# Performance work log

Hardware: AMD Instinct MI355X
Metric: run time of the kernel (lower is better)

## Reference

```python
import jax, jax.numpy as jnp
from jax import lax
import numpy as np

T, B, I, H, L = 512, 256, 512, 256, 2  # seq, batch, input, hidden, layers per stack


def _param_shapes():
    # (stack, layer) -> input dim of that layer. Stack1 layer0 sees I, everything else sees H.
    shapes = []
    for s, in0 in enumerate([I, H]):
        for l in range(L):
            d_in = in0 if l == 0 else H
            shapes.append((f"s{s+1}l{l}", d_in))
    return shapes


def setup_inputs() -> dict:
    key = jax.random.key(0)
    d = {"x": jax.random.normal(jax.random.fold_in(key, 0), (T, B, I), jnp.float32)}
    k = 1.0 / np.sqrt(H)  # pytorch LSTM init scale
    i = 1
    for name, d_in in _param_shapes():
        d[name + "_wih"] = jax.random.uniform(jax.random.fold_in(key, i + 0), (4 * H, d_in), jnp.float32, -k, k)
        d[name + "_whh"] = jax.random.uniform(jax.random.fold_in(key, i + 1), (4 * H, H), jnp.float32, -k, k)
        d[name + "_bih"] = jax.random.uniform(jax.random.fold_in(key, i + 2), (4 * H,), jnp.float32, -k, k)
        d[name + "_bhh"] = jax.random.uniform(jax.random.fold_in(key, i + 3), (4 * H,), jnp.float32, -k, k)
        i += 4
    d["lr_w"] = jax.random.uniform(jax.random.fold_in(key, 100), (H, H), jnp.float32, -k, k)
    d["lr_b"] = jax.random.uniform(jax.random.fold_in(key, 101), (H,), jnp.float32, -k, k)
    return d


def _lstm_layer(x, wih, whh, bih, bhh):
    # x: (T, B, d_in) -> (T, B, H). PyTorch gate order: i, f, g, o.
    xg = jnp.einsum("tbi,gi->tbg", x, wih) + bih + bhh  # precompute input proj (T, B, 4H)
    h0 = jnp.zeros((x.shape[1], H), x.dtype)

    def step(carry, xt):
        h, c = carry
        g = xt + h @ whh.T
        gi, gf, gg, go = jnp.split(g, 4, axis=-1)
        c = jax.nn.sigmoid(gf) * c + jax.nn.sigmoid(gi) * jnp.tanh(gg)
        h = jax.nn.sigmoid(go) * jnp.tanh(c)
        return (h, c), h

    _, ys = lax.scan(step, (h0, h0), xg)
    return ys


def _forward(x, params, lr_w, lr_b):
    out = x
    for (wih, whh, bih, bhh) in params:
        out = _lstm_layer(out, wih, whh, bih, bhh)
    out = out @ lr_w.T + lr_b  # (T, B, H)
    return out[:, -1]  # faithful to original: index dim 1 (batch dim) -> (T, H)


def reference(x,
              s1l0_wih, s1l0_whh, s1l0_bih, s1l0_bhh,
              s1l1_wih, s1l1_whh, s1l1_bih, s1l1_bhh,
              s2l0_wih, s2l0_whh, s2l0_bih, s2l0_bhh,
              s2l1_wih, s2l1_whh, s2l1_bih, s2l1_bhh,
              lr_w, lr_b):
    params = [
        (s1l0_wih, s1l0_whh, s1l0_bih, s1l0_bhh),
        (s1l1_wih, s1l1_whh, s1l1_bih, s1l1_bhh),
        (s2l0_wih, s2l0_whh, s2l0_bih, s2l0_bhh),
        (s2l1_wih, s2l1_whh, s2l1_bih, s2l1_bhh),
    ]
    return _forward(x, params, lr_w, lr_b)
```

## Files before the change

### kernel.cpp

```cpp
#include <hip/hip_runtime.h>
#include <stdint.h>


typedef _Float16 half2v __attribute__((ext_vector_type(2)));

__device__ __forceinline__ float fdot2u(uint32_t w, uint32_t h, float acc) {
#if __has_builtin(__builtin_amdgcn_fdot2)
  return __builtin_amdgcn_fdot2(__builtin_bit_cast(half2v, w),
                                __builtin_bit_cast(half2v, h), acc, false);
#else
  half2v wv = __builtin_bit_cast(half2v, w);
  half2v hv = __builtin_bit_cast(half2v, h);
  acc += (float)wv[0] * (float)hv[0];
  acc += (float)wv[1] * (float)hv[1];
  return acc;
#endif
}

__device__ __forceinline__ float sigmoidf_(float x) {
  return 1.f / (1.f + __expf(-x));
}
__device__ __forceinline__ float tanhf_(float x) {
  return 1.f - 2.f / (__expf(2.f * x) + 1.f);
}

#define CNT_STRIDE 32

__device__ __forceinline__ int cnt_load(const int* p) {
  return __hip_atomic_load(p, __ATOMIC_RELAXED, __HIP_MEMORY_SCOPE_AGENT);
}
__device__ __forceinline__ void cnt_store(int* p, int v) {
  __hip_atomic_store(p, v, __ATOMIC_RELAXED, __HIP_MEMORY_SCOPE_AGENT);
}
__device__ __forceinline__ float ldg_f32(const float* p) {
  uint32_t u = __hip_atomic_load((const uint32_t*)p, __ATOMIC_RELAXED,
                                 __HIP_MEMORY_SCOPE_AGENT);
  return __builtin_bit_cast(float, u);
}
__device__ __forceinline__ void stg_f32(float* p, float v) {
  __hip_atomic_store((uint32_t*)p, __builtin_bit_cast(uint32_t, v),
                     __ATOMIC_RELAXED, __HIP_MEMORY_SCOPE_AGENT);
}
__device__ __forceinline__ uint64_t ldg_u64(const float* p) {
  return __hip_atomic_load((const uint64_t*)p, __ATOMIC_RELAXED,
                           __HIP_MEMORY_SCOPE_AGENT);
}

__device__ __forceinline__ void wait_ge(const int* p, int need, int& rdy) {
  while (rdy < need) {
    rdy = cnt_load(p);
    if (rdy < need) __builtin_amdgcn_s_sleep(2);
  }
  asm volatile("" ::: "memory");
}

__global__ void zero_cnt(int* c) {
  if (threadIdx.x < 16 * CNT_STRIDE) c[threadIdx.x] = 0;
}

__global__ __launch_bounds__(256) void pack_whh(const float* __restrict__ w,
                                                uint32_t* __restrict__ wpk) {
  int idx = blockIdx.x * 256 + threadIdx.x;
  int r = idx >> 7, k2 = idx & 127;
  float f0 = w[r * 256 + 2 * k2];
  float f1 = w[r * 256 + 2 * k2 + 1];
  union { _Float16 h; uint16_t u; } a, b;
  a.h = (_Float16)f0;
  b.h = (_Float16)f1;
  wpk[idx] = (uint32_t)a.u | ((uint32_t)b.u << 16);
}

__global__ __launch_bounds__(256) void proj_gemm(const float* __restrict__ in, int istride, int K,
                                                 const float* __restrict__ W,
                                                 const float* __restrict__ bih,
                                                 const float* __restrict__ bhh,
                                                 float* __restrict__ xg) {
  __shared__ float xs[8][512];
  const int tid = threadIdx.x;
  const int r = blockIdx.x * 256 + tid;
  const int t0 = blockIdx.y * 8;
  for (int tt = 0; tt < 8; ++tt)
    for (int k = tid; k < K; k += 256)
      xs[tt][k] = in[(size_t)(t0 + tt) * istride + k];
  __syncthreads();
  float bias = bih[r] + bhh[r];
  float acc[8];
#pragma unroll
  for (int j = 0; j < 8; ++j) acc[j] = bias;
  const float* wr = W + (size_t)r * K;
  for (int k = 0; k < K; k += 4) {
    float4 w4 = *reinterpret_cast<const float4*>(wr + k);
#pragma unroll
    for (int j = 0; j < 8; ++j)
      acc[j] += xs[j][k] * w4.x + xs[j][k + 1] * w4.y + xs[j][k + 2] * w4.z +
                xs[j][k + 3] * w4.w;
  }
#pragma unroll
  for (int j = 0; j < 8; ++j) xg[(size_t)(t0 + j) * 1024 + r] = acc[j];
}


__device__ void scan_fn(int l, const uint32_t* __restrict__ wpk,
                        const float* __restrict__ xgsrc,
                        float* __restrict__ hseq, int* __restrict__ cnt) {
  __shared__ __align__(16) uint4 wlds[8 * 2 * 512];
  __shared__ __align__(16) uint16_t hbuf[2][256];
  const int tid = threadIdx.x;
  const int j = tid >> 1;
  const int odd = tid & 1;
  const int rA = j + (odd ? 512 : 0);
  const int rB = rA + 256;

  uint32_t wA[96], wB[96];
  {
    const uint4* gA = reinterpret_cast<const uint4*>(wpk + rA * 128);
    const uint4* gB = reinterpret_cast<const uint4*>(wpk + rB * 128);
#pragma unroll
    for (int q = 0; q < 24; ++q) {
      uint4 a = gA[q];
      wA[4 * q + 0] = a.x; wA[4 * q + 1] = a.y; wA[4 * q + 2] = a.z; wA[4 * q + 3] = a.w;
      uint4 b = gB[q];
      wB[4 * q + 0] = b.x; wB[4 * q + 1] = b.y; wB[4 * q + 2] = b.z; wB[4 * q + 3] = b.w;
    }
#pragma unroll
    for (int c = 0; c < 8; ++c) {
      wlds[(c * 2 + 0) * 512 + tid] = gA[24 + c];
      wlds[(c * 2 + 1) * 512 + tid] = gB[24 + c];
    }
  }
  if (tid < 256) hbuf[0][tid] = 0;
  __syncthreads();

  const int* mycnt = &cnt[(4 + (l - 1) * 2 + odd) * CNT_STRIDE];
  int rdy = 0;
  if (l) wait_ge(mycnt, 1, rdy);
  float c_ = 0.f;
  float xga = ldg_f32(xgsrc + rA), xgb = ldg_f32(xgsrc + rB);
  int pp = 0;
  for (int t = 0; t < 512; ++t) {
    const int tn = (t < 511) ? (t + 1) : 511;
    if (l) {
      int need = (t + 2 > 512) ? 512 : (t + 2);
      wait_ge(mycnt, need, rdy);
    }
    float nxa = ldg_f32(xgsrc + tn * 1024 + rA);
    float nxb = ldg_f32(xgsrc + tn * 1024 + rB);

    float accA0 = xga, accA1 = 0.f, accB0 = xgb, accB1 = 0.f;
    const uint4* hv4 = reinterpret_cast<const uint4*>(&hbuf[pp][0]);
#pragma unroll
    for (int ch = 0; ch < 24; ++ch) {
      uint4 h4 = hv4[ch];
      accA0 = fdot2u(wA[4 * ch + 0], h4.x, accA0);
      accA1 = fdot2u(wA[4 * ch + 1], h4.y, accA1);
      accA0 = fdot2u(wA[4 * ch + 2], h4.z, accA0);
      accA1 = fdot2u(wA[4 * ch + 3], h4.w, accA1);
      accB0 = fdot2u(wB[4 * ch + 0], h4.x, accB0);
      accB1 = fdot2u(wB[4 * ch + 1], h4.y, accB1);
      accB0 = fdot2u(wB[4 * ch + 2], h4.z, accB0);
      accB1 = fdot2u(wB[4 * ch + 3], h4.w, accB1);
    }
#pragma unroll
    for (int cc = 0; cc < 8; ++cc) {
      uint4 h4 = hv4[24 + cc];
      uint4 wa = wlds[(cc * 2 + 0) * 512 + tid];
      uint4 wb = wlds[(cc * 2 + 1) * 512 + tid];
      accA0 = fdot2u(wa.x, h4.x, accA0);
      accA1 = fdot2u(wa.y, h4.y, accA1);
      accA0 = fdot2u(wa.z, h4.z, accA0);
      accA1 = fdot2u(wa.w, h4.w, accA1);
      accB0 = fdot2u(wb.x, h4.x, accB0);
      accB1 = fdot2u(wb.y, h4.y, accB1);
      accB0 = fdot2u(wb.z, h4.z, accB0);
      accB1 = fdot2u(wb.w, h4.w, accB1);
    }
    float accA = accA0 + accA1;
    float accB = accB0 + accB1;

    float o0 = __shfl_xor(accA, 1);
    float o1 = __shfl_xor(accB, 1);
    float pi = odd ? o0 : accA;
    float pf = odd ? o1 : accB;
    float pg = odd ? accA : o0;
    float po = odd ? accB : o1;

    c_ = sigmoidf_(pf) * c_ + sigmoidf_(pi) * tanhf_(pg);
    float h = sigmoidf_(po) * tanhf_(c_);
    if (!odd) {
      stg_f32(hseq + t * 256 + j, h);
      union { _Float16 hf; uint16_t u; } cv;
      cv.hf = (_Float16)h;
      hbuf[pp ^ 1][j] = cv.u;
    }
    __syncthreads();
    if (tid == 0) cnt_store(&cnt[l * CNT_STRIDE], t + 1);
    pp ^= 1;
    xga = nxa;
    xgb = nxb;
  }
}

__device__ void proj_fn(int l, int half, const uint32_t* __restrict__ wpk,
                        const float* __restrict__ bih, const float* __restrict__ bhh,
                        const float* __restrict__ hsrc,
                        float* __restrict__ xgdst, int* __restrict__ cnt) {
  __shared__ __align__(16) uint32_t hpk[128];
  const int tid = threadIdx.x;
  const int row = half * 512 + tid;

  uint32_t wr_[128];
  {
    const uint4* g = reinterpret_cast<const uint4*>(wpk + (size_t)row * 128);
#pragma unroll
    for (int q = 0; q < 32; ++q) {
      uint4 v = g[q];
      wr_[4 * q + 0] = v.x; wr_[4 * q + 1] = v.y; wr_[4 * q + 2] = v.z; wr_[4 * q + 3] = v.w;
    }
  }
  const float bias = bih[row] + bhh[row];
  const int* prev = &cnt[(l - 1) * CNT_STRIDE];
  int* mine = &cnt[(4 + (l - 1) * 2 + half) * CNT_STRIDE];
  int rdy = 0;

  for (int t = 0; t < 512; ++t) {
    wait_ge(prev, t + 1, rdy);
    if (tid < 128) {
      uint64_t hv = ldg_u64(hsrc + t * 256 + 2 * tid);
      float hx = __builtin_bit_cast(float, (uint32_t)hv);
      float hy = __builtin_bit_cast(float, (uint32_t)(hv >> 32));
      union { _Float16 h; uint16_t u; } a, b;
      a.h = (_Float16)hx;
      b.h = (_Float16)hy;
      hpk[tid] = (uint32_t)a.u | ((uint32_t)b.u << 16);
    }
    __syncthreads();
    float a0 = bias, a1 = 0.f;
    const uint4* hv4 = reinterpret_cast<const uint4*>(hpk);
#pragma unroll
    for (int q = 0; q < 32; ++q) {
      uint4 h4 = hv4[q];
      a0 = fdot2u(wr_[4 * q + 0], h4.x, a0);
      a1 = fdot2u(wr_[4 * q + 1], h4.y, a1);
      a0 = fdot2u(wr_[4 * q + 2], h4.z, a0);
      a1 = fdot2u(wr_[4 * q + 3], h4.w, a1);
    }
    stg_f32(xgdst + t * 1024 + row, a0 + a1);
    __syncthreads();
    if (tid == 0) cnt_store(mine, t + 1);
  }
}

__global__ __launch_bounds__(512, 2) void pipeline(
    const uint32_t* __restrict__ wpkhh, const uint32_t* __restrict__ wpkih,
    const float* __restrict__ xg0, float* __restrict__ xgp,
    float* __restrict__ hseq,
    const float* __restrict__ bih1, const float* __restrict__ bhh1,
    const float* __restrict__ bih2, const float* __restrict__ bhh2,
    const float* __restrict__ bih3, const float* __restrict__ bhh3,
    int* __restrict__ cnt) {
  const int bx = blockIdx.x;
  if (bx == 0) {
    scan_fn(0, wpkhh, xg0, hseq, cnt);
  } else {
    const int g = bx - 1;
    const int l = g / 3 + 1;
    const int r = g % 3;
    const float* bih = (l == 1) ? bih1 : (l == 2) ? bih2 : bih3;
    const float* bhh = (l == 1) ? bhh1 : (l == 2) ? bhh2 : bhh3;
    if (r < 2)
      proj_fn(l, r, wpkih + (size_t)(l - 1) * 131072, bih, bhh,
              hseq + (size_t)(l - 1) * 131072, xgp + (size_t)(l - 1) * 524288, cnt);
    else
      scan_fn(l, wpkhh + (size_t)l * 131072, xgp + (size_t)(l - 1) * 524288,
              hseq + (size_t)l * 131072, cnt);
  }
}

__global__ __launch_bounds__(256) void final_gemm(const float* __restrict__ h3,
                                                  const float* __restrict__ lrw,
                                                  const float* __restrict__ lrb,
                                                  float* __restrict__ out) {
  __shared__ float xs[8][256];
  const int j = threadIdx.x;
  const int t0 = blockIdx.x * 8;
  for (int tt = 0; tt < 8; ++tt) xs[tt][j] = h3[(t0 + tt) * 256 + j];
  __syncthreads();
  float bias = lrb[j];
  float acc[8];
#pragma unroll
  for (int jj = 0; jj < 8; ++jj) acc[jj] = bias;
  const float* wr = lrw + j * 256;
  for (int k = 0; k < 256; k += 4) {
    float4 w4 = *reinterpret_cast<const float4*>(wr + k);
#pragma unroll
    for (int jj = 0; jj < 8; ++jj)
      acc[jj] += xs[jj][k] * w4.x + xs[jj][k + 1] * w4.y + xs[jj][k + 2] * w4.z +
                 xs[jj][k + 3] * w4.w;
  }
#pragma unroll
  for (int jj = 0; jj < 8; ++jj) out[(t0 + jj) * 256 + j] = acc[jj];
}

extern "C" void kernel_launch(void* const* d_in, const int* in_sizes, int n_in,
                              void* d_out, int out_size, void* d_ws, size_t ws_size,
                              hipStream_t stream) {
  (void)in_sizes; (void)n_in; (void)out_size; (void)ws_size;
  const float* x = (const float*)d_in[0];
  const float* wih[4] = {(const float*)d_in[1], (const float*)d_in[5],
                         (const float*)d_in[9], (const float*)d_in[13]};
  const float* whh[4] = {(const float*)d_in[2], (const float*)d_in[6],
                         (const float*)d_in[10], (const float*)d_in[14]};
  const float* bih[4] = {(const float*)d_in[3], (const float*)d_in[7],
                         (const float*)d_in[11], (const float*)d_in[15]};
  const float* bhh[4] = {(const float*)d_in[4], (const float*)d_in[8],
                         (const float*)d_in[12], (const float*)d_in[16]};
  const float* lrw = (const float*)d_in[17];
  const float* lrb = (const float*)d_in[18];
  float* out = (float*)d_out;

  float* ws = (float*)d_ws;
  float* xg0 = ws;
  float* xgp = ws + 524288;
  float* hseq = xgp + 3 * 524288;
  uint32_t* wpkhh = (uint32_t*)(hseq + 4 * 131072);
  uint32_t* wpkih = wpkhh + 4 * 131072;
  int* cnt = (int*)(wpkih + 3 * 131072);

  zero_cnt<<<1, 512, 0, stream>>>(cnt);
  for (int l = 0; l < 4; ++l)
    pack_whh<<<512, 256, 0, stream>>>(whh[l], wpkhh + (size_t)l * 131072);
  for (int l = 1; l < 4; ++l)
    pack_whh<<<512, 256, 0, stream>>>(wih[l], wpkih + (size_t)(l - 1) * 131072);

  proj_gemm<<<dim3(4, 64), 256, 0, stream>>>(x + 255 * 512, 256 * 512, 512,
                                             wih[0], bih[0], bhh[0], xg0);

  pipeline<<<10, 512, 0, stream>>>(wpkhh, wpkih, xg0, xgp, hseq,
                                   bih[1], bhh[1], bih[2], bhh[2], bih[3], bhh[3],
                                   cnt);

  final_gemm<<<64, 256, 0, stream>>>(hseq + 3 * 131072, lrw, lrb, out);
}
```

Measured before the change: 1.176 ms.

## Fuse final linear into pipeline, batch projection steps by four, merge pack kernels

Merges the seven weight-pack launches into one kernel that picks its source matrix by block index. Projection blocks now wait for four timesteps at a time and compute four outputs per synchronisation, which cuts counter polling and barrier overhead. The final linear layer moves into an extra pipeline block that consumes the last layer's hidden states as they are produced, so it overlaps the scan instead of running after it. The cost is more latency between a scan step and its consumer, and one more persistent block spinning on counters.

```diff
diff --git a/kernel.cpp b/kernel.cpp
--- a/kernel.cpp
+++ b/kernel.cpp
@@ -58,16 +58,24 @@
   if (threadIdx.x < 16 * CNT_STRIDE) c[threadIdx.x] = 0;
 }
 
-__global__ __launch_bounds__(256) void pack_whh(const float* __restrict__ w,
-                                                uint32_t* __restrict__ wpk) {
-  int idx = blockIdx.x * 256 + threadIdx.x;
+__global__ __launch_bounds__(256) void pack_all(
+    const float* __restrict__ w0, const float* __restrict__ w1,
+    const float* __restrict__ w2, const float* __restrict__ w3,
+    const float* __restrict__ w4, const float* __restrict__ w5,
+    const float* __restrict__ w6, uint32_t* __restrict__ dst) {
+  int b = blockIdx.x;
+  int m = b >> 9;
+  const float* src = (m == 0) ? w0 : (m == 1) ? w1 : (m == 2) ? w2
+                   : (m == 3) ? w3 : (m == 4) ? w4 : (m == 5) ? w5 : w6;
+  uint32_t* d = dst + (size_t)m * 131072;
+  int idx = (b & 511) * 256 + threadIdx.x;
   int r = idx >> 7, k2 = idx & 127;
-  float f0 = w[r * 256 + 2 * k2];
-  float f1 = w[r * 256 + 2 * k2 + 1];
-  union { _Float16 h; uint16_t u; } a, b;
+  float f0 = src[r * 256 + 2 * k2];
+  float f1 = src[r * 256 + 2 * k2 + 1];
+  union { _Float16 h; uint16_t u; } a, bb;
   a.h = (_Float16)f0;
-  b.h = (_Float16)f1;
-  wpk[idx] = (uint32_t)a.u | ((uint32_t)b.u << 16);
+  bb.h = (_Float16)f1;
+  d[idx] = (uint32_t)a.u | ((uint32_t)bb.u << 16);
 }
 
 __global__ __launch_bounds__(256) void proj_gemm(const float* __restrict__ in, int istride, int K,
@@ -204,7 +212,7 @@
                         const float* __restrict__ bih, const float* __restrict__ bhh,
                         const float* __restrict__ hsrc,
                         float* __restrict__ xgdst, int* __restrict__ cnt) {
-  __shared__ __align__(16) uint32_t hpk[128];
+  __shared__ __align__(16) uint32_t hpk[4][128];
   const int tid = threadIdx.x;
   const int row = half * 512 + tid;
 
@@ -221,32 +229,79 @@
   const int* prev = &cnt[(l - 1) * CNT_STRIDE];
   int* mine = &cnt[(4 + (l - 1) * 2 + half) * CNT_STRIDE];
   int rdy = 0;
-
-  for (int t = 0; t < 512; ++t) {
-    wait_ge(prev, t + 1, rdy);
-    if (tid < 128) {
-      uint64_t hv = ldg_u64(hsrc + t * 256 + 2 * tid);
+  const int s4 = tid >> 7;
+  const int c4 = tid & 127;
+
+  for (int tt = 0; tt < 128; ++tt) {
+    const int t0 = tt * 4;
+    wait_ge(prev, t0 + 4, rdy);
+    {
+      uint64_t hv = ldg_u64(hsrc + (t0 + s4) * 256 + 2 * c4);
       float hx = __builtin_bit_cast(float, (uint32_t)hv);
       float hy = __builtin_bit_cast(float, (uint32_t)(hv >> 32));
       union { _Float16 h; uint16_t u; } a, b;
       a.h = (_Float16)hx;
       b.h = (_Float16)hy;
-      hpk[tid] = (uint32_t)a.u | ((uint32_t)b.u << 16);
-    }
-    __syncthreads();
-    float a0 = bias, a1 = 0.f;
-    const uint4* hv4 = reinterpret_cast<const uint4*>(hpk);
+      hpk[s4][c4] = (uint32_t)a.u | ((uint32_t)b.u << 16);
+    }
+    __syncthreads();
+#pragma unroll
+    for (int s = 0; s < 4; ++s) {
+      float a0 = bias, a1 = 0.f;
+      const uint4* hv4 = reinterpret_cast<const uint4*>(hpk[s]);
+#pragma unroll
+      for (int q = 0; q < 32; ++q) {
+        uint4 h4 = hv4[q];
+        a0 = fdot2u(wr_[4 * q + 0], h4.x, a0);
+        a1 = fdot2u(wr_[4 * q + 1], h4.y, a1);
+        a0 = fdot2u(wr_[4 * q + 2], h4.z, a0);
+        a1 = fdot2u(wr_[4 * q + 3], h4.w, a1);
+      }
+      stg_f32(xgdst + (t0 + s) * 1024 + row, a0 + a1);
+    }
+    __syncthreads();
+    if (tid == 0) cnt_store(mine, t0 + 4);
+  }
+}
+
+__device__ void final_fn(const float* __restrict__ lrw, const float* __restrict__ lrb,
+                         const float* __restrict__ h3, float* __restrict__ out,
+                         const int* __restrict__ cnt) {
+  __shared__ __align__(16) float hs[256];
+  const int tid = threadIdx.x;
+  const int row = tid >> 1;
+  const int kh = tid & 1;
+  float w_[128];
+  {
+    const float4* g = reinterpret_cast<const float4*>(lrw + (size_t)row * 256 + kh * 128);
 #pragma unroll
     for (int q = 0; q < 32; ++q) {
-      uint4 h4 = hv4[q];
-      a0 = fdot2u(wr_[4 * q + 0], h4.x, a0);
-      a1 = fdot2u(wr_[4 * q + 1], h4.y, a1);
-      a0 = fdot2u(wr_[4 * q + 2], h4.z, a0);
-      a1 = fdot2u(wr_[4 * q + 3], h4.w, a1);
-    }
-    stg_f32(xgdst + t * 1024 + row, a0 + a1);
-    __syncthreads();
-    if (tid == 0) cnt_store(mine, t + 1);
+      float4 v = g[q];
+      w_[4 * q + 0] = v.x; w_[4 * q + 1] = v.y; w_[4 * q + 2] = v.z; w_[4 * q + 3] = v.w;
+    }
+  }
+  const float bias = lrb[row];
+  const int* prev = &cnt[3 * CNT_STRIDE];
+  int rdy = 0;
+  for (int t = 0; t < 512; ++t) {
+    wait_ge(prev, t + 1, rdy);
+    if (tid < 128) {
+      uint64_t hv = ldg_u64(h3 + t * 256 + 2 * tid);
+      hs[2 * tid] = __builtin_bit_cast(float, (uint32_t)hv);
+      hs[2 * tid + 1] = __builtin_bit_cast(float, (uint32_t)(hv >> 32));
+    }
+    __syncthreads();
+    float a0 = 0.f, a1 = 0.f;
+    const float* hp = hs + kh * 128;
+#pragma unroll
+    for (int k = 0; k < 128; k += 4) {
+      a0 += w_[k] * hp[k] + w_[k + 2] * hp[k + 2];
+      a1 += w_[k + 1] * hp[k + 1] + w_[k + 3] * hp[k + 3];
+    }
+    float s = a0 + a1;
+    s += __shfl_xor(s, 1);
+    if (!kh) out[t * 256 + row] = s + bias;
+    __syncthreads();
   }
 }
 
@@ -257,10 +312,13 @@
     const float* __restrict__ bih1, const float* __restrict__ bhh1,
     const float* __restrict__ bih2, const float* __restrict__ bhh2,
     const float* __restrict__ bih3, const float* __restrict__ bhh3,
-    int* __restrict__ cnt) {
+    const float* __restrict__ lrw, const float* __restrict__ lrb,
+    float* __restrict__ out, int* __restrict__ cnt) {
   const int bx = blockIdx.x;
   if (bx == 0) {
     scan_fn(0, wpkhh, xg0, hseq, cnt);
+  } else if (bx == 10) {
+    final_fn(lrw, lrb, hseq + (size_t)3 * 131072, out, cnt);
   } else {
     const int g = bx - 1;
     const int l = g / 3 + 1;
@@ -274,31 +332,6 @@
       scan_fn(l, wpkhh + (size_t)l * 131072, xgp + (size_t)(l - 1) * 524288,
               hseq + (size_t)l * 131072, cnt);
   }
-}
-
-__global__ __launch_bounds__(256) void final_gemm(const float* __restrict__ h3,
-                                                  const float* __restrict__ lrw,
-                                                  const float* __restrict__ lrb,
-                                                  float* __restrict__ out) {
-  __shared__ float xs[8][256];
-  const int j = threadIdx.x;
-  const int t0 = blockIdx.x * 8;
-  for (int tt = 0; tt < 8; ++tt) xs[tt][j] = h3[(t0 + tt) * 256 + j];
-  __syncthreads();
-  float bias = lrb[j];
-  float acc[8];
-#pragma unroll
-  for (int jj = 0; jj < 8; ++jj) acc[jj] = bias;
-  const float* wr = lrw + j * 256;
-  for (int k = 0; k < 256; k += 4) {
-    float4 w4 = *reinterpret_cast<const float4*>(wr + k);
-#pragma unroll
-    for (int jj = 0; jj < 8; ++jj)
-      acc[jj] += xs[jj][k] * w4.x + xs[jj][k + 1] * w4.y + xs[jj][k + 2] * w4.z +
-                 xs[jj][k + 3] * w4.w;
-  }
-#pragma unroll
-  for (int jj = 0; jj < 8; ++jj) out[(t0 + jj) * 256 + j] = acc[jj];
 }
 
 extern "C" void kernel_launch(void* const* d_in, const int* in_sizes, int n_in,
@@ -327,17 +360,13 @@
   int* cnt = (int*)(wpkih + 3 * 131072);
 
   zero_cnt<<<1, 512, 0, stream>>>(cnt);
-  for (int l = 0; l < 4; ++l)
-    pack_whh<<<512, 256, 0, stream>>>(whh[l], wpkhh + (size_t)l * 131072);
-  for (int l = 1; l < 4; ++l)
-    pack_whh<<<512, 256, 0, stream>>>(wih[l], wpkih + (size_t)(l - 1) * 131072);
+  pack_all<<<3584, 256, 0, stream>>>(whh[0], whh[1], whh[2], whh[3],
+                                     wih[1], wih[2], wih[3], wpkhh);
 
   proj_gemm<<<dim3(4, 64), 256, 0, stream>>>(x + 255 * 512, 256 * 512, 512,
                                              wih[0], bih[0], bhh[0], xg0);
 
-  pipeline<<<10, 512, 0, stream>>>(wpkhh, wpkih, xg0, xgp, hseq,
+  pipeline<<<11, 512, 0, stream>>>(wpkhh, wpkih, xg0, xgp, hseq,
                                    bih[1], bhh[1], bih[2], bhh[2], bih[3], bhh[3],
-                                   cnt);
-
-  final_gemm<<<64, 256, 0, stream>>>(hseq + 3 * 131072, lrw, lrb, out);
-}
+                                   lrw, lrb, out, cnt);
+}
```

Result: no change. 1.167 ms (-0.7%).
